# Performance work log

Hardware: AMD Instinct MI355X
Metric: run time of the kernel (lower is better)

The kernel has to match this reference:

```python
import jax, jax.numpy as jnp
import numpy as np
from jax import lax

H_SP, W_SP = 32, 8   # idx == 0
NUM_HEADS = 2
DIM = 64
SCALE = (DIM // NUM_HEADS) ** -0.5


def conv1x1(x, w, b):
    # x: [B,C,H,W], w: [O,C,1,1], b: [O]
    return jnp.einsum('bchw,oc->bohw', x, w[:, :, 0, 0]) + b[None, :, None, None]


def dwconv5(x, w, b):
    # depthwise 5x5, pad 2. w: [C,1,5,5]
    y = lax.conv_general_dilated(
        x, w, window_strides=(1, 1), padding=[(2, 2), (2, 2)],
        dimension_numbers=('NCHW', 'OIHW', 'NCHW'),
        feature_group_count=x.shape[1])
    return y + b[None, :, None, None]


def im2cswin(x):
    # [B,C,H,W] -> [B*nH*nW, heads, H_SP*W_SP, C//heads]
    B, C, H, W = x.shape
    x = x.reshape(B, C, H // H_SP, H_SP, W // W_SP, W_SP)
    x = x.transpose(0, 2, 4, 3, 5, 1).reshape(-1, H_SP * W_SP, NUM_HEADS, C // NUM_HEADS)
    return x.transpose(0, 2, 1, 3)


def windows2img(xw, H, W):
    # [B', H_SP*W_SP, C] -> [B, C, H, W]
    B = xw.shape[0] // ((H // H_SP) * (W // W_SP))
    x = xw.reshape(B, H // H_SP, W // W_SP, H_SP, W_SP, -1)
    return x.transpose(0, 5, 1, 3, 2, 4).reshape(B, -1, H, W)


def setup_inputs() -> dict:
    key = jax.random.key(0)
    ks = jax.random.split(key, 8)
    B, C, H, W = 4, DIM, 256, 256
    s = 0.02
    return {
        'x': jax.random.normal(ks[0], (B, C, H, W), dtype=jnp.float32),
        'qk_w': jax.random.normal(ks[1], (2 * C, C, 1, 1), dtype=jnp.float32) * s,
        'qk_b': jnp.zeros((2 * C,), jnp.float32),
        'q5_w': jax.random.normal(ks[2], (C, 1, 5, 5), dtype=jnp.float32) * s,
        'q5_b': jnp.zeros((C,), jnp.float32),
        'k5_w': jax.random.normal(ks[3], (C, 1, 5, 5), dtype=jnp.float32) * s,
        'k5_b': jnp.zeros((C,), jnp.float32),
        'v_w': jax.random.normal(ks[4], (C, C, 1, 1), dtype=jnp.float32) * s,
        'v_b': jnp.zeros((C,), jnp.float32),
        'lepe_w': jax.random.normal(ks[5], (C, 1, 5, 5), dtype=jnp.float32) * s,
        'lepe_b': jnp.zeros((C,), jnp.float32),
    }


def reference(x, qk_w, qk_b, q5_w, q5_b, k5_w, k5_b, v_w, v_b, lepe_w, lepe_b):
    B, C, H, W = x.shape
    pad_r = (W_SP - W % W_SP) % W_SP
    pad_b = (H_SP - H % H_SP) % H_SP
    xp = jnp.pad(x, ((0, 0), (0, 0), (0, pad_b), (0, pad_r)))
    Hp, Wp = xp.shape[2], xp.shape[3]
    # shift_size == 0 -> no roll
    qk = conv1x1(xp, qk_w, qk_b)
    q, k = jnp.split(qk, 2, axis=1)
    v = conv1x1(xp, v_w, v_b)
    lepe = dwconv5(v, lepe_w, lepe_b)
    qw = im2cswin(dwconv5(q, q5_w, q5_b) + lepe)   # [nw, h, N, d]
    kw = im2cswin(dwconv5(k, k5_w, k5_b) + lepe)
    vw = im2cswin(v)
    attn = jnp.einsum('whnd,whmd->whnm', qw * SCALE, kw)
    attn = jax.nn.softmax(attn, axis=-1)
    out = jnp.einsum('whnm,whmd->whnd', attn, vw)
    out = out.transpose(0, 2, 1, 3).reshape(-1, H_SP * W_SP, C)
    out = windows2img(out, Hp, Wp) + lepe
    if pad_r or pad_b:
        out = out[:, :, :H, :W]
    return out
```

## Files before the change

kernel.cpp:

```cpp
#include <hip/hip_runtime.h>


typedef unsigned short u16;
typedef short s16x8 __attribute__((ext_vector_type(8)));
typedef float f32x4 __attribute__((ext_vector_type(4)));

#define MFMA16(a, b, c) __builtin_amdgcn_mfma_f32_16x16x32_bf16((a), (b), (c), 0, 0, 0)

#define SCALE_F 0.17677669529663687f
#define LOG2E_F 1.4426950408889634f

#if __has_builtin(__builtin_amdgcn_exp2f)
#define EXP2F(x) __builtin_amdgcn_exp2f(x)
#else
#define EXP2F(x) exp2f(x)
#endif

#if __has_builtin(__builtin_amdgcn_rcpf)
#define RCPF(x) __builtin_amdgcn_rcpf(x)
#else
#define RCPF(x) (1.f / (x))
#endif

#if __has_builtin(__builtin_amdgcn_fdot2_f32_bf16)
#define HAVE_DOT2 1
typedef __bf16 bf16x2_t __attribute__((ext_vector_type(2)));
__device__ __forceinline__ float dot2bf(unsigned a, unsigned b, float c) {
  return __builtin_amdgcn_fdot2_f32_bf16(__builtin_bit_cast(bf16x2_t, a),
                                         __builtin_bit_cast(bf16x2_t, b), c,
                                         false);
}
#else
#define HAVE_DOT2 0
#endif

__device__ __forceinline__ u16 f2bf(float f) {
  unsigned u = __float_as_uint(f);
  return (u16)((u + 0x7FFFu + ((u >> 16) & 1u)) >> 16);
}
__device__ __forceinline__ float bf2f(u16 h) {
  return __uint_as_float(((unsigned)h) << 16);
}
__device__ __forceinline__ unsigned pk_rne(float lo, float hi) {
  unsigned ul = __float_as_uint(lo), uh = __float_as_uint(hi);
  ul += 0x7FFFu + ((ul >> 16) & 1u);
  uh += 0x7FFFu + ((uh >> 16) & 1u);
  return (ul >> 16) | (uh & 0xFFFF0000u);
}

__global__ __launch_bounds__(256, 4) void k1_conv1x1(
    const float* __restrict__ x, const float* __restrict__ qk_w,
    const float* __restrict__ qk_b, const float* __restrict__ v_w,
    const float* __restrict__ v_b, u16* __restrict__ qkv) {
  __shared__ u16 Wl[12288];
  __shared__ float Bl[192];
  int t = threadIdx.x;
  for (int i = t; i < 12288; i += 256) {
    int oc = i >> 6, ic = i & 63;
    float wv_ = (oc < 128) ? qk_w[i] : v_w[i - 8192];
    Wl[(oc << 6) | (ic ^ ((oc & 7) << 3))] = f2bf(wv_);
  }
  if (t < 192) Bl[t] = (t < 128) ? qk_b[t] : v_b[t - 128];
  __syncthreads();

  int lane = t & 63, wv = t >> 6;
  int col = lane & 15, g = lane >> 4;
  int p0 = blockIdx.x * 64 + wv * 16;
  int b = p0 >> 16, pix0 = p0 & 65535;

  const float* xb = x + (size_t)b * 4194304 + pix0 + col;
  s16x8 bfrag[2];
#pragma unroll
  for (int kk = 0; kk < 2; ++kk) {
#pragma unroll
    for (int j = 0; j < 8; ++j) {
      int ic = kk * 32 + g * 8 + j;
      bfrag[kk][j] = (short)f2bf(xb[(size_t)ic << 16]);
    }
  }

  f32x4 acc[12];
#pragma unroll
  for (int mt = 0; mt < 12; ++mt) acc[mt] = 0.f;
#pragma unroll
  for (int mt = 0; mt < 12; ++mt) {
    int oc = mt * 16 + col;
    int swz = (oc & 7) << 3;
#pragma unroll
    for (int kk = 0; kk < 2; ++kk) {
      s16x8 af = *(const s16x8*)&Wl[(oc << 6) | ((kk * 32 + g * 8) ^ swz)];
      acc[mt] = MFMA16(af, bfrag[kk], acc[mt]);
    }
  }

  u16* ob = qkv + (size_t)b * 12582912 + pix0 + col;
#pragma unroll
  for (int mt = 0; mt < 12; ++mt) {
#pragma unroll
    for (int r = 0; r < 4; ++r) {
      int oc = mt * 16 + g * 4 + r;
      ob[(size_t)oc << 16] = f2bf(acc[mt][r] + Bl[oc]);
    }
  }
}


__device__ __forceinline__ int qt_off(int tok, int d) {
  return (tok << 5) + (d ^ (((tok >> 2) & 3) << 3));
}
__device__ __forceinline__ int vt_off(int d, int tok) {
  int swz = (((d & 7) ^ ((tok >> 6) & 3)) << 3);
  return (d << 8) + ((tok & ~7) ^ swz) + (tok & 7);
}

template <bool WANTC>
__device__ __forceinline__ void conv25(const u16* hb, const unsigned* ww,
                                       float* acc, unsigned& cA, unsigned& cB) {
#pragma unroll
  for (int i = 0; i < 5; ++i) {
    uint2 A = *(const uint2*)&hb[i * 12];
    uint2 Bv = *(const uint2*)&hb[i * 12 + 4];
    if (WANTC && i == 2) {
      cA = A.y;
      cB = Bv.x;
    }
#if HAVE_DOT2
    unsigned o1 = (A.x >> 16) | (A.y << 16);
    unsigned o3 = (A.y >> 16) | (Bv.x << 16);
    unsigned o5 = (Bv.x >> 16) | (Bv.y << 16);
    unsigned o7 = (Bv.y >> 16) | (Bv.y << 16);
    unsigned pr[8] = {A.x, o1, A.y, o3, Bv.x, o5, Bv.y, o7};
#pragma unroll
    for (int j = 0; j < 4; ++j) {
      float a0 = dot2bf(pr[j], ww[i * 3], acc[j]);
      a0 = dot2bf(pr[j + 2], ww[i * 3 + 1], a0);
      acc[j] = dot2bf(pr[j + 4], ww[i * 3 + 2], a0);
    }
#else
    float px[8];
    px[0] = __uint_as_float(A.x << 16);
    px[1] = __uint_as_float(A.x & 0xffff0000u);
    px[2] = __uint_as_float(A.y << 16);
    px[3] = __uint_as_float(A.y & 0xffff0000u);
    px[4] = __uint_as_float(Bv.x << 16);
    px[5] = __uint_as_float(Bv.x & 0xffff0000u);
    px[6] = __uint_as_float(Bv.y << 16);
    px[7] = __uint_as_float(Bv.y & 0xffff0000u);
    float w5[5];
    w5[0] = __uint_as_float(ww[i * 3] << 16);
    w5[1] = __uint_as_float(ww[i * 3] & 0xffff0000u);
    w5[2] = __uint_as_float(ww[i * 3 + 1] << 16);
    w5[3] = __uint_as_float(ww[i * 3 + 1] & 0xffff0000u);
    w5[4] = __uint_as_float(ww[i * 3 + 2] << 16);
#pragma unroll
    for (int jj = 0; jj < 5; ++jj)
#pragma unroll
      for (int j = 0; j < 4; ++j) acc[j] = fmaf(px[j + jj], w5[jj], acc[j]);
#endif
  }
}

__global__ __launch_bounds__(512, 4) void k23_fused(
    const u16* __restrict__ qkv, const float* __restrict__ q5_w,
    const float* __restrict__ q5_b, const float* __restrict__ k5_w,
    const float* __restrict__ k5_b, const float* __restrict__ lepe_w,
    const float* __restrict__ lepe_b, float* __restrict__ out) {
  __shared__ u16 SM[40256];
  u16* QT = SM;
  u16* KT = SM + 8192;
  u16* VT = SM + 16384;
  u16* LT = SM + 24576;
  u16* HS = SM + 32768;
  unsigned* WLp = (unsigned*)(SM + 36224);
  float* BLf = (float*)(SM + 40064);

  int raw = blockIdx.x;
  int bid = (raw & 7) * 256 + (raw >> 3);
  int head = bid & 1, wj = (bid >> 1) & 31, wi = (bid >> 6) & 7, b = bid >> 9;
  int h0 = wi * 32, w0 = wj * 8;

  int t = threadIdx.x;
  int wv = t >> 6, lane = t & 63;
  int dl = lane & 7, tq = lane >> 3;
  const size_t bbase = (size_t)b * 12582912;

  for (int i = t; i < 1440; i += 512) {
    int ts = i / 480, rem = i - ts * 480, ch = rem / 15, rk = rem - ch * 15;
    int r = rk / 3, k2 = rk - r * 3;
    const float* srcw = (ts == 0 ? lepe_w : ts == 1 ? q5_w : k5_w) +
                        (head * 32 + ch) * 25 + r * 5 + k2 * 2;
    float lo = srcw[0];
    float hi = (k2 < 2) ? srcw[1] : 0.f;
    WLp[ts * 640 + ch * 20 + rk] = pk_rne(lo, hi);
  }
  if (t < 96) {
    int ts = t >> 5, ch = t & 31;
    BLf[t] = (ts == 0 ? lepe_b : ts == 1 ? q5_b : k5_b)[head * 32 + ch];
  }

  unsigned fixOff[4], okm[4];
  int ldsOff[4];
  bool live[4];
#pragma unroll
  for (int it = 0; it < 4; ++it) {
    int ip = t + it * 512;
    live[it] = ip < 1728;
    int ipc = live[it] ? ip : 0;
    int ch = ipc / 216, rem = ipc - ch * 216;
    int hr = rem / 6, hc = rem - hr * 6;
    int gh = h0 - 2 + hr, gw = w0 - 2 + hc * 2;
    bool ok = live[it] & ((unsigned)gh < 256u) & ((unsigned)gw <= 254u);
    int hcl = gh < 0 ? 0 : (gh > 255 ? 255 : gh);
    int wcl = gw < 0 ? 0 : (gw > 254 ? 254 : gw);
    fixOff[it] = ((unsigned)ch << 16) + hcl * 256 + wcl;
    okm[it] = ok ? 0xffffffffu : 0u;
    ldsOff[it] = (ch * 36 + hr) * 12 + hc * 2;
  }

  unsigned crV[4], crQ[4], crK[4];
  auto stage_ld = [&](int p, unsigned* cr) {
    int cg = p / 3, ts = p - cg * 3;
    int planeBase = (ts == 0 ? 128 : ts == 1 ? 0 : 64) + head * 32 + cg * 8;
    const u16* src = qkv + bbase + ((size_t)planeBase << 16);
#pragma unroll
    for (int it = 0; it < 4; ++it)
      if (live[it]) {
        unsigned v = *(const unsigned*)&src[fixOff[it]];
        cr[it] = v & okm[it];
      }
  };
  auto stage_st = [&](const unsigned* cr) {
#pragma unroll
    for (int it = 0; it < 4; ++it)
      if (live[it]) *(unsigned*)&HS[ldsOff[it]] = cr[it];
  };

  stage_ld(0, crV);
  stage_st(crV);
  stage_ld(1, crQ);
  stage_ld(2, crK);
  stage_ld(3, crV);
  __syncthreads();

  int row = wv * 4 + (tq >> 1), c0 = (tq & 1) * 4;
  int tok0 = wv * 32 + tq * 4;
  int hq = tq >> 2;
  int sBv = wv * 32 + (tq & 3) * 8 + hq * 4;
  int qjb = (dl & 1) ? 2 : 0;
  const u16* hb = &HS[(dl * 36 + row) * 12 + c0];
  float lepA[4];

  auto loadw = [&](int ts, int d, unsigned* ww) {
    const uint4* wp = (const uint4*)(WLp + ts * 640 + d * 20);
    uint4 a = wp[0], b4 = wp[1], c4 = wp[2], e4 = wp[3];
    ww[0] = a.x; ww[1] = a.y; ww[2] = a.z; ww[3] = a.w;
    ww[4] = b4.x; ww[5] = b4.y; ww[6] = b4.z; ww[7] = b4.w;
    ww[8] = c4.x; ww[9] = c4.y; ww[10] = c4.z; ww[11] = c4.w;
    ww[12] = e4.x; ww[13] = e4.y; ww[14] = e4.z;
  };

  auto do_qk = [&](const unsigned* ww, float bias, u16* tile, bool doScale,
                   int d) {
    float acc[4] = {bias, bias, bias, bias};
    unsigned du0, du1;
    conv25<false>(hb, ww, acc, du0, du1);
    float o0 = acc[0] + lepA[0], o1 = acc[1] + lepA[1];
    float o2 = acc[2] + lepA[2], o3 = acc[3] + lepA[3];
    if (doScale) {
      o0 *= SCALE_F;
      o1 *= SCALE_F;
      o2 *= SCALE_F;
      o3 *= SCALE_F;
    }
    unsigned q01 = pk_rne(o0, o1), q23 = pk_rne(o2, o3);
    unsigned sendq = (dl & 1) ? q01 : q23;
    unsigned recvq = (unsigned)__shfl_xor((int)sendq, 1);
    unsigned aQ = (dl & 1) ? recvq : q01;
    unsigned bQ = (dl & 1) ? q23 : recvq;
    unsigned wlo = (aQ & 0xffffu) | (bQ << 16);
    unsigned whi = (aQ >> 16) | (bQ & 0xffff0000u);
    int dp = d & ~1;
    unsigned* tw = (unsigned*)tile;
    int wq0 = ((tok0 + qjb) << 4) + ((dp ^ ((tq & 3) << 3)) >> 1);
    tw[wq0] = wlo;
    tw[wq0 + 16] = whi;
  };

#pragma unroll 1
  for (int cg = 0; cg < 4; ++cg) {
    int d = cg * 8 + dl;
    unsigned ww[16];
    loadw(0, d, ww);
    {
      float bias = BLf[d];
      float acc[4] = {bias, bias, bias, bias};
      unsigned cA, cB;
      conv25<true>(hb, ww, acc, cA, cB);
      uint2 ol;
      ol.x = pk_rne(acc[0], acc[1]);
      ol.y = pk_rne(acc[2], acc[3]);
      *(uint2*)&LT[vt_off(d, tok0)] = ol;
      unsigned sendv = hq ? cA : cB;
      unsigned recvv = (unsigned)__shfl_xor((int)sendv, 32);
      unsigned aW = hq ? recvv : cA;
      unsigned bW = hq ? cB : recvv;
      uint2 ov;
      ov.x = (aW & 0xffffu) | (bW << 16);
      ov.y = (aW >> 16) | (bW & 0xffff0000u);
      *(uint2*)&VT[vt_off(d, sBv)] = ov;
#pragma unroll
      for (int j = 0; j < 4; ++j) lepA[j] = acc[j];
    }
    __syncthreads();
    stage_st(crQ);
    if (cg < 3) stage_ld(cg * 3 + 4, crQ);
    __syncthreads();
    loadw(1, d, ww);
    do_qk(ww, BLf[32 + d], QT, true, d);
    __syncthreads();
    stage_st(crK);
    if (cg < 3) stage_ld(cg * 3 + 5, crK);
    __syncthreads();
    loadw(2, d, ww);
    do_qk(ww, BLf[64 + d], KT, false, d);
    __syncthreads();
    if (cg < 3) {
      stage_st(crV);
      if (cg < 2) stage_ld(cg * 3 + 6, crV);
      __syncthreads();
    }
  }

  int col = lane & 15, g = lane >> 4;
  int rbase = wv * 32;

  s16x8 qa[2];
  float lepr[2][8];
#pragma unroll
  for (int mt = 0; mt < 2; ++mt) {
    int tok = rbase + mt * 16 + col;
    qa[mt] = *(const s16x8*)&QT[qt_off(tok, g * 8)];
#pragma unroll
    for (int dt = 0; dt < 2; ++dt)
#pragma unroll
      for (int r = 0; r < 4; ++r) {
        int d = dt * 16 + g * 4 + r;
        lepr[mt][dt * 4 + r] = bf2f(LT[vt_off(d, tok)]);
      }
  }
  __syncthreads();

  u16* Pw = (wv < 4) ? (SM + wv * 2048) : (SM + 24576 + (wv - 4) * 2048);
  float* ob = out + (((size_t)(b * 64 + head * 32)) << 16) + h0 * 256 + w0;

#pragma unroll 1
  for (int mt = 0; mt < 2; ++mt) {
    int row0 = rbase + mt * 16;
    f32x4 zero = 0.f;
    f32x4 sacc[16];
    __builtin_amdgcn_s_setprio(1);
#pragma unroll
    for (int nt = 0; nt < 16; ++nt) {
      int tj = nt * 16 + col;
      s16x8 kb = *(const s16x8*)&KT[qt_off(tj, g * 8)];
      sacc[nt] = MFMA16(qa[mt], kb, zero);
    }
    __builtin_amdgcn_s_setprio(0);
    unsigned pw[4][8];
    float ssum[4];
#pragma unroll
    for (int r = 0; r < 4; ++r) {
      float pv[16];
#pragma unroll
      for (int nt = 0; nt < 16; ++nt) pv[nt] = EXP2F(sacc[nt][r]);
      float s0 = 0.f;
#if HAVE_DOT2
#pragma unroll
      for (int w = 0; w < 8; ++w) {
        pw[r][w] = pk_rne(pv[2 * w], pv[2 * w + 1]);
        s0 = dot2bf(pw[r][w], 0x3F803F80u, s0);
      }
#else
#pragma unroll
      for (int w = 0; w < 8; ++w) {
        pw[r][w] = pk_rne(pv[2 * w], pv[2 * w + 1]);
        s0 += pv[2 * w] + pv[2 * w + 1];
      }
#endif
#pragma unroll
      for (int s = 1; s < 16; s <<= 1) s0 += __shfl_xor(s0, s);
      ssum[r] = s0;
    }
    int srcl = (col >> 2) << 4;
    float t0 = __shfl(ssum[0], srcl);
    float t1 = __shfl(ssum[1], srcl);
    float t2 = __shfl(ssum[2], srcl);
    float t3 = __shfl(ssum[3], srcl);
    float sA = (col & 1) ? t1 : t0;
    float sB = (col & 1) ? t3 : t2;
    float inv = RCPF((col & 2) ? sB : sA);

    f32x4 oacc[2];
    oacc[0] = 0.f;
    oacc[1] = 0.f;
    unsigned* PwU = (unsigned*)Pw;
#pragma unroll
    for (int chunk = 0; chunk < 2; ++chunk) {
#pragma unroll
      for (int r = 0; r < 4; ++r) {
        int irow = g * 4 + r;
        int wb = irow * 64;
        int sw = (irow & 7) << 2;
#pragma unroll
        for (int al = 0; al < 4; ++al)
          PwU[wb + ((al * 16 + col) ^ sw)] = pw[r][chunk * 4 + al];
      }
      __builtin_amdgcn_s_setprio(1);
#pragma unroll
      for (int ks = 0; ks < 4; ++ks) {
        int kcp = (ks * 16 + g * 4) ^ ((col & 7) << 2);
        s16x8 pb = *(const s16x8*)&PwU[col * 64 + kcp];
        int sig = chunk * 128 + ks * 32 + g * 8;
#pragma unroll
        for (int dt = 0; dt < 2; ++dt) {
          s16x8 va = *(const s16x8*)&VT[vt_off(dt * 16 + col, sig)];
          oacc[dt] = MFMA16(va, pb, oacc[dt]);
        }
      }
      __builtin_amdgcn_s_setprio(0);
    }
    int tok = row0 + col;
#pragma unroll
    for (int dt = 0; dt < 2; ++dt) {
#pragma unroll
      for (int r = 0; r < 4; ++r) {
        int d = dt * 16 + g * 4 + r;
        float val = fmaf(oacc[dt][r], inv, lepr[mt][dt * 4 + r]);
        ob[((size_t)d << 16) + (tok >> 3) * 256 + (tok & 7)] = val;
      }
    }
  }
}

extern "C" void kernel_launch(void* const* d_in, const int* in_sizes, int n_in,
                              void* d_out, int out_size, void* d_ws,
                              size_t ws_size, hipStream_t stream) {
  const float* x = (const float*)d_in[0];
  const float* qk_w = (const float*)d_in[1];
  const float* qk_b = (const float*)d_in[2];
  const float* q5_w = (const float*)d_in[3];
  const float* q5_b = (const float*)d_in[4];
  const float* k5_w = (const float*)d_in[5];
  const float* k5_b = (const float*)d_in[6];
  const float* v_w = (const float*)d_in[7];
  const float* v_b = (const float*)d_in[8];
  const float* lepe_w = (const float*)d_in[9];
  const float* lepe_b = (const float*)d_in[10];
  float* out = (float*)d_out;

  if (ws_size < 100663296ull) return;
  u16* qkv = (u16*)d_ws;

  hipLaunchKernelGGL(k1_conv1x1, dim3(4096), dim3(256), 0, stream, x, qk_w,
                     qk_b, v_w, v_b, qkv);
  hipLaunchKernelGGL(k23_fused, dim3(2048), dim3(512), 0, stream, qkv, q5_w,
                     q5_b, k5_w, k5_b, lepe_w, lepe_b, out);
}
```

Measured before the change: 202.7 us.

## Process two horizontally adjacent windows per block and merge their output stores

```diff
diff --git a/kernel.cpp b/kernel.cpp
--- a/kernel.cpp
+++ b/kernel.cpp
@@ -175,9 +175,9 @@
   float* BLf = (float*)(SM + 40064);
 
   int raw = blockIdx.x;
-  int bid = (raw & 7) * 256 + (raw >> 3);
-  int head = bid & 1, wj = (bid >> 1) & 31, wi = (bid >> 6) & 7, b = bid >> 9;
-  int h0 = wi * 32, w0 = wj * 8;
+  int bid = (raw & 7) * 128 + (raw >> 3);
+  int head = bid & 1, wj2 = (bid >> 1) & 15, wi = (bid >> 5) & 7, b = bid >> 8;
+  int h0 = wi * 32, w0A = wj2 * 16;
 
   int t = threadIdx.x;
   int wv = t >> 6, lane = t & 63;
@@ -198,9 +198,9 @@
     BLf[t] = (ts == 0 ? lepe_b : ts == 1 ? q5_b : k5_b)[head * 32 + ch];
   }
 
-  unsigned fixOff[4], okm[4];
-  int ldsOff[4];
-  bool live[4];
+  unsigned ch16[4];
+  int hcs[4], ldsOff[4];
+  bool live[4], okh[4];
 #pragma unroll
   for (int it = 0; it < 4; ++it) {
     int ip = t + it * 512;
@@ -208,39 +208,13 @@
     int ipc = live[it] ? ip : 0;
     int ch = ipc / 216, rem = ipc - ch * 216;
     int hr = rem / 6, hc = rem - hr * 6;
-    int gh = h0 - 2 + hr, gw = w0 - 2 + hc * 2;
-    bool ok = live[it] & ((unsigned)gh < 256u) & ((unsigned)gw <= 254u);
+    int gh = h0 - 2 + hr;
+    okh[it] = live[it] & ((unsigned)gh < 256u);
     int hcl = gh < 0 ? 0 : (gh > 255 ? 255 : gh);
-    int wcl = gw < 0 ? 0 : (gw > 254 ? 254 : gw);
-    fixOff[it] = ((unsigned)ch << 16) + hcl * 256 + wcl;
-    okm[it] = ok ? 0xffffffffu : 0u;
+    ch16[it] = ((unsigned)ch << 16) + hcl * 256;
+    hcs[it] = hc;
     ldsOff[it] = (ch * 36 + hr) * 12 + hc * 2;
   }
-
-  unsigned crV[4], crQ[4], crK[4];
-  auto stage_ld = [&](int p, unsigned* cr) {
-    int cg = p / 3, ts = p - cg * 3;
-    int planeBase = (ts == 0 ? 128 : ts == 1 ? 0 : 64) + head * 32 + cg * 8;
-    const u16* src = qkv + bbase + ((size_t)planeBase << 16);
-#pragma unroll
-    for (int it = 0; it < 4; ++it)
-      if (live[it]) {
-        unsigned v = *(const unsigned*)&src[fixOff[it]];
-        cr[it] = v & okm[it];
-      }
-  };
-  auto stage_st = [&](const unsigned* cr) {
-#pragma unroll
-    for (int it = 0; it < 4; ++it)
-      if (live[it]) *(unsigned*)&HS[ldsOff[it]] = cr[it];
-  };
-
-  stage_ld(0, crV);
-  stage_st(crV);
-  stage_ld(1, crQ);
-  stage_ld(2, crK);
-  stage_ld(3, crV);
-  __syncthreads();
 
   int row = wv * 4 + (tq >> 1), c0 = (tq & 1) * 4;
   int tok0 = wv * 32 + tq * 4;
@@ -248,7 +222,10 @@
   int sBv = wv * 32 + (tq & 3) * 8 + hq * 4;
   int qjb = (dl & 1) ? 2 : 0;
   const u16* hb = &HS[(dl * 36 + row) * 12 + c0];
-  float lepA[4];
+  int col = lane & 15, g = lane >> 4;
+  int rbase = wv * 32;
+  u16* Pw = (wv < 4) ? (SM + wv * 2048) : (SM + 24576 + (wv - 4) * 2048);
+  float* obA = out + (((size_t)(b * 64 + head * 32)) << 16) + h0 * 256 + w0A;
 
   auto loadw = [&](int ts, int d, unsigned* ww) {
     const uint4* wp = (const uint4*)(WLp + ts * 640 + d * 20);
@@ -259,184 +236,230 @@
     ww[12] = e4.x; ww[13] = e4.y; ww[14] = e4.z;
   };
 
-  auto do_qk = [&](const unsigned* ww, float bias, u16* tile, bool doScale,
-                   int d) {
-    float acc[4] = {bias, bias, bias, bias};
-    unsigned du0, du1;
-    conv25<false>(hb, ww, acc, du0, du1);
-    float o0 = acc[0] + lepA[0], o1 = acc[1] + lepA[1];
-    float o2 = acc[2] + lepA[2], o3 = acc[3] + lepA[3];
-    if (doScale) {
-      o0 *= SCALE_F;
-      o1 *= SCALE_F;
-      o2 *= SCALE_F;
-      o3 *= SCALE_F;
-    }
-    unsigned q01 = pk_rne(o0, o1), q23 = pk_rne(o2, o3);
-    unsigned sendq = (dl & 1) ? q01 : q23;
-    unsigned recvq = (unsigned)__shfl_xor((int)sendq, 1);
-    unsigned aQ = (dl & 1) ? recvq : q01;
-    unsigned bQ = (dl & 1) ? q23 : recvq;
-    unsigned wlo = (aQ & 0xffffu) | (bQ << 16);
-    unsigned whi = (aQ >> 16) | (bQ & 0xffff0000u);
-    int dp = d & ~1;
-    unsigned* tw = (unsigned*)tile;
-    int wq0 = ((tok0 + qjb) << 4) + ((dp ^ ((tq & 3) << 3)) >> 1);
-    tw[wq0] = wlo;
-    tw[wq0 + 16] = whi;
-  };
+  float h0v[8], h1v[8];
 
 #pragma unroll 1
-  for (int cg = 0; cg < 4; ++cg) {
-    int d = cg * 8 + dl;
-    unsigned ww[16];
-    loadw(0, d, ww);
-    {
-      float bias = BLf[d];
+  for (int win = 0; win < 2; ++win) {
+    int w0 = w0A + win * 8;
+
+    unsigned fixOff[4], okm[4];
+#pragma unroll
+    for (int it = 0; it < 4; ++it) {
+      int gw = w0 - 2 + hcs[it] * 2;
+      bool ok = okh[it] & ((unsigned)gw <= 254u);
+      int wcl = gw < 0 ? 0 : (gw > 254 ? 254 : gw);
+      fixOff[it] = ch16[it] + wcl;
+      okm[it] = ok ? 0xffffffffu : 0u;
+    }
+
+    unsigned crV[4], crQ[4], crK[4];
+    auto stage_ld = [&](int p, unsigned* cr) {
+      int cg = p / 3, ts = p - cg * 3;
+      int planeBase = (ts == 0 ? 128 : ts == 1 ? 0 : 64) + head * 32 + cg * 8;
+      const u16* src = qkv + bbase + ((size_t)planeBase << 16);
+#pragma unroll
+      for (int it = 0; it < 4; ++it)
+        if (live[it]) {
+          unsigned v = *(const unsigned*)&src[fixOff[it]];
+          cr[it] = v & okm[it];
+        }
+    };
+    auto stage_st = [&](const unsigned* cr) {
+#pragma unroll
+      for (int it = 0; it < 4; ++it)
+        if (live[it]) *(unsigned*)&HS[ldsOff[it]] = cr[it];
+    };
+
+    stage_ld(0, crV);
+    stage_st(crV);
+    stage_ld(1, crQ);
+    stage_ld(2, crK);
+    stage_ld(3, crV);
+    __syncthreads();
+
+    float lepA[4];
+    auto do_qk = [&](const unsigned* ww, float bias, u16* tile, bool doScale,
+                     int d) {
       float acc[4] = {bias, bias, bias, bias};
-      unsigned cA, cB;
-      conv25<true>(hb, ww, acc, cA, cB);
-      uint2 ol;
-      ol.x = pk_rne(acc[0], acc[1]);
-      ol.y = pk_rne(acc[2], acc[3]);
-      *(uint2*)&LT[vt_off(d, tok0)] = ol;
-      unsigned sendv = hq ? cA : cB;
-      unsigned recvv = (unsigned)__shfl_xor((int)sendv, 32);
-      unsigned aW = hq ? recvv : cA;
-      unsigned bW = hq ? cB : recvv;
-      uint2 ov;
-      ov.x = (aW & 0xffffu) | (bW << 16);
-      ov.y = (aW >> 16) | (bW & 0xffff0000u);
-      *(uint2*)&VT[vt_off(d, sBv)] = ov;
-#pragma unroll
-      for (int j = 0; j < 4; ++j) lepA[j] = acc[j];
+      unsigned du0, du1;
+      conv25<false>(hb, ww, acc, du0, du1);
+      float o0 = acc[0] + lepA[0], o1 = acc[1] + lepA[1];
+      float o2 = acc[2] + lepA[2], o3 = acc[3] + lepA[3];
+      if (doScale) {
+        o0 *= SCALE_F;
+        o1 *= SCALE_F;
+        o2 *= SCALE_F;
+        o3 *= SCALE_F;
+      }
+      unsigned q01 = pk_rne(o0, o1), q23 = pk_rne(o2, o3);
+      unsigned sendq = (dl & 1) ? q01 : q23;
+      unsigned recvq = (unsigned)__shfl_xor((int)sendq, 1);
+      unsigned aQ = (dl & 1) ? recvq : q01;
+      unsigned bQ = (dl & 1) ? q23 : recvq;
+      unsigned wlo = (aQ & 0xffffu) | (bQ << 16);
+      unsigned whi = (aQ >> 16) | (bQ & 0xffff0000u);
+      int dp = d & ~1;
+      unsigned* tw = (unsigned*)tile;
+      int wq0 = ((tok0 + qjb) << 4) + ((dp ^ ((tq & 3) << 3)) >> 1);
+      tw[wq0] = wlo;
+      tw[wq0 + 16] = whi;
+    };
+
+#pragma unroll 1
+    for (int cg = 0; cg < 4; ++cg) {
+      int d = cg * 8 + dl;
+      unsigned ww[16];
+      loadw(0, d, ww);
+      {
+        float bias = BLf[d];
+        float acc[4] = {bias, bias, bias, bias};
+        unsigned cA, cB;
+        conv25<true>(hb, ww, acc, cA, cB);
+        uint2 ol;
+        ol.x = pk_rne(acc[0], acc[1]);
+        ol.y = pk_rne(acc[2], acc[3]);
+        *(uint2*)&LT[vt_off(d, tok0)] = ol;
+        unsigned sendv = hq ? cA : cB;
+        unsigned recvv = (unsigned)__shfl_xor((int)sendv, 32);
+        unsigned aW = hq ? recvv : cA;
+        unsigned bW = hq ? cB : recvv;
+        uint2 ov;
+        ov.x = (aW & 0xffffu) | (bW << 16);
+        ov.y = (aW >> 16) | (bW & 0xffff0000u);
+        *(uint2*)&VT[vt_off(d, sBv)] = ov;
+#pragma unroll
+        for (int j = 0; j < 4; ++j) lepA[j] = acc[j];
+      }
+      __syncthreads();
+      stage_st(crQ);
+      if (cg < 3) stage_ld(cg * 3 + 4, crQ);
+      __syncthreads();
+      loadw(1, d, ww);
+      do_qk(ww, BLf[32 + d], QT, true, d);
+      __syncthreads();
+      stage_st(crK);
+      if (cg < 3) stage_ld(cg * 3 + 5, crK);
+      __syncthreads();
+      loadw(2, d, ww);
+      do_qk(ww, BLf[64 + d], KT, false, d);
+      __syncthreads();
+      if (cg < 3) {
+        stage_st(crV);
+        if (cg < 2) stage_ld(cg * 3 + 6, crV);
+        __syncthreads();
+      }
+    }
+
+    s16x8 qa[2];
+    float lepr[2][8];
+#pragma unroll
+    for (int mt = 0; mt < 2; ++mt) {
+      int tok = rbase + mt * 16 + col;
+      qa[mt] = *(const s16x8*)&QT[qt_off(tok, g * 8)];
+#pragma unroll
+      for (int dt = 0; dt < 2; ++dt)
+#pragma unroll
+        for (int r = 0; r < 4; ++r) {
+          int d = dt * 16 + g * 4 + r;
+          lepr[mt][dt * 4 + r] = bf2f(LT[vt_off(d, tok)]);
+        }
     }
     __syncthreads();
-    stage_st(crQ);
-    if (cg < 3) stage_ld(cg * 3 + 4, crQ);
-    __syncthreads();
-    loadw(1, d, ww);
-    do_qk(ww, BLf[32 + d], QT, true, d);
-    __syncthreads();
-    stage_st(crK);
-    if (cg < 3) stage_ld(cg * 3 + 5, crK);
-    __syncthreads();
-    loadw(2, d, ww);
-    do_qk(ww, BLf[64 + d], KT, false, d);
-    __syncthreads();
-    if (cg < 3) {
-      stage_st(crV);
-      if (cg < 2) stage_ld(cg * 3 + 6, crV);
-      __syncthreads();
-    }
-  }
-
-  int col = lane & 15, g = lane >> 4;
-  int rbase = wv * 32;
-
-  s16x8 qa[2];
-  float lepr[2][8];
-#pragma unroll
-  for (int mt = 0; mt < 2; ++mt) {
-    int tok = rbase + mt * 16 + col;
-    qa[mt] = *(const s16x8*)&QT[qt_off(tok, g * 8)];
-#pragma unroll
-    for (int dt = 0; dt < 2; ++dt)
+
+#pragma unroll 1
+    for (int mt = 0; mt < 2; ++mt) {
+      f32x4 zero = 0.f;
+      f32x4 sacc[16];
+      __builtin_amdgcn_s_setprio(1);
+#pragma unroll
+      for (int nt = 0; nt < 16; ++nt) {
+        int tj = nt * 16 + col;
+        s16x8 kb = *(const s16x8*)&KT[qt_off(tj, g * 8)];
+        sacc[nt] = MFMA16(qa[mt], kb, zero);
+      }
+      __builtin_amdgcn_s_setprio(0);
+      unsigned pw[4][8];
+      float ssum[4];
 #pragma unroll
       for (int r = 0; r < 4; ++r) {
-        int d = dt * 16 + g * 4 + r;
-        lepr[mt][dt * 4 + r] = bf2f(LT[vt_off(d, tok)]);
-      }
-  }
-  __syncthreads();
-
-  u16* Pw = (wv < 4) ? (SM + wv * 2048) : (SM + 24576 + (wv - 4) * 2048);
-  float* ob = out + (((size_t)(b * 64 + head * 32)) << 16) + h0 * 256 + w0;
-
-#pragma unroll 1
-  for (int mt = 0; mt < 2; ++mt) {
-    int row0 = rbase + mt * 16;
-    f32x4 zero = 0.f;
-    f32x4 sacc[16];
-    __builtin_amdgcn_s_setprio(1);
-#pragma unroll
-    for (int nt = 0; nt < 16; ++nt) {
-      int tj = nt * 16 + col;
-      s16x8 kb = *(const s16x8*)&KT[qt_off(tj, g * 8)];
-      sacc[nt] = MFMA16(qa[mt], kb, zero);
-    }
-    __builtin_amdgcn_s_setprio(0);
-    unsigned pw[4][8];
-    float ssum[4];
-#pragma unroll
-    for (int r = 0; r < 4; ++r) {
-      float pv[16];
-#pragma unroll
-      for (int nt = 0; nt < 16; ++nt) pv[nt] = EXP2F(sacc[nt][r]);
-      float s0 = 0.f;
+        float pv[16];
+#pragma unroll
+        for (int nt = 0; nt < 16; ++nt) pv[nt] = EXP2F(sacc[nt][r]);
+        float s0 = 0.f;
 #if HAVE_DOT2
 #pragma unroll
-      for (int w = 0; w < 8; ++w) {
-        pw[r][w] = pk_rne(pv[2 * w], pv[2 * w + 1]);
-        s0 = dot2bf(pw[r][w], 0x3F803F80u, s0);
-      }
+        for (int w = 0; w < 8; ++w) {
+          pw[r][w] = pk_rne(pv[2 * w], pv[2 * w + 1]);
+          s0 = dot2bf(pw[r][w], 0x3F803F80u, s0);
+        }
 #else
 #pragma unroll
-      for (int w = 0; w < 8; ++w) {
-        pw[r][w] = pk_rne(pv[2 * w], pv[2 * w + 1]);
-        s0 += pv[2 * w] + pv[2 * w + 1];
-      }
+        for (int w = 0; w < 8; ++w) {
+          pw[r][w] = pk_rne(pv[2 * w], pv[2 * w + 1]);
+          s0 += pv[2 * w] + pv[2 * w + 1];
+        }
 #endif
 #pragma unroll
-      for (int s = 1; s < 16; s <<= 1) s0 += __shfl_xor(s0, s);
-      ssum[r] = s0;
-    }
-    int srcl = (col >> 2) << 4;
-    float t0 = __shfl(ssum[0], srcl);
-    float t1 = __shfl(ssum[1], srcl);
-    float t2 = __shfl(ssum[2], srcl);
-    float t3 = __shfl(ssum[3], srcl);
-    float sA = (col & 1) ? t1 : t0;
-    float sB = (col & 1) ? t3 : t2;
-    float inv = RCPF((col & 2) ? sB : sA);
-
-    f32x4 oacc[2];
-    oacc[0] = 0.f;
-    oacc[1] = 0.f;
-    unsigned* PwU = (unsigned*)Pw;
-#pragma unroll
-    for (int chunk = 0; chunk < 2; ++chunk) {
-#pragma unroll
-      for (int r = 0; r < 4; ++r) {
-        int irow = g * 4 + r;
-        int wb = irow * 64;
-        int sw = (irow & 7) << 2;
-#pragma unroll
-        for (int al = 0; al < 4; ++al)
-          PwU[wb + ((al * 16 + col) ^ sw)] = pw[r][chunk * 4 + al];
-      }
-      __builtin_amdgcn_s_setprio(1);
-#pragma unroll
-      for (int ks = 0; ks < 4; ++ks) {
-        int kcp = (ks * 16 + g * 4) ^ ((col & 7) << 2);
-        s16x8 pb = *(const s16x8*)&PwU[col * 64 + kcp];
-        int sig = chunk * 128 + ks * 32 + g * 8;
-#pragma unroll
-        for (int dt = 0; dt < 2; ++dt) {
-          s16x8 va = *(const s16x8*)&VT[vt_off(dt * 16 + col, sig)];
-          oacc[dt] = MFMA16(va, pb, oacc[dt]);
-        }
-      }
-      __builtin_amdgcn_s_setprio(0);
-    }
-    int tok = row0 + col;
-#pragma unroll
-    for (int dt = 0; dt < 2; ++dt) {
-#pragma unroll
-      for (int r = 0; r < 4; ++r) {
-        int d = dt * 16 + g * 4 + r;
-        float val = fmaf(oacc[dt][r], inv, lepr[mt][dt * 4 + r]);
-        ob[((size_t)d << 16) + (tok >> 3) * 256 + (tok & 7)] = val;
+        for (int s = 1; s < 16; s <<= 1) s0 += __shfl_xor(s0, s);
+        ssum[r] = s0;
+      }
+      int srcl = (col >> 2) << 4;
+      float t0 = __shfl(ssum[0], srcl);
+      float t1 = __shfl(ssum[1], srcl);
+      float t2 = __shfl(ssum[2], srcl);
+      float t3 = __shfl(ssum[3], srcl);
+      float sA = (col & 1) ? t1 : t0;
+      float sB = (col & 1) ? t3 : t2;
+      float inv = RCPF((col & 2) ? sB : sA);
+
+      f32x4 oacc[2];
+      oacc[0] = 0.f;
+      oacc[1] = 0.f;
+      unsigned* PwU = (unsigned*)Pw;
+#pragma unroll
+      for (int chunk = 0; chunk < 2; ++chunk) {
+#pragma unroll
+        for (int r = 0; r < 4; ++r) {
+          int irow = g * 4 + r;
+          int wb = irow * 64;
+          int sw = (irow & 7) << 2;
+#pragma unroll
+          for (int al = 0; al < 4; ++al)
+            PwU[wb + ((al * 16 + col) ^ sw)] = pw[r][chunk * 4 + al];
+        }
+        __builtin_amdgcn_s_setprio(1);
+#pragma unroll
+        for (int ks = 0; ks < 4; ++ks) {
+          int kcp = (ks * 16 + g * 4) ^ ((col & 7) << 2);
+          s16x8 pb = *(const s16x8*)&PwU[col * 64 + kcp];
+          int sig = chunk * 128 + ks * 32 + g * 8;
+#pragma unroll
+          for (int dt = 0; dt < 2; ++dt) {
+            s16x8 va = *(const s16x8*)&VT[vt_off(dt * 16 + col, sig)];
+            oacc[dt] = MFMA16(va, pb, oacc[dt]);
+          }
+        }
+        __builtin_amdgcn_s_setprio(0);
+      }
+      int tok = rbase + mt * 16 + col;
+#pragma unroll
+      for (int dt = 0; dt < 2; ++dt) {
+#pragma unroll
+        for (int r = 0; r < 4; ++r) {
+          int d = dt * 16 + g * 4 + r;
+          float val = fmaf(oacc[dt][r], inv, lepr[mt][dt * 4 + r]);
+          if (win == 0) {
+            if (mt == 0)
+              h0v[dt * 4 + r] = val;
+            else
+              h1v[dt * 4 + r] = val;
+          } else {
+            float hv = (mt == 0) ? h0v[dt * 4 + r] : h1v[dt * 4 + r];
+            size_t off = ((size_t)d << 16) + (tok >> 3) * 256 + (tok & 7);
+            obA[off] = hv;
+            obA[off + 8] = val;
+          }
+        }
       }
     }
   }
@@ -463,6 +486,6 @@
 
   hipLaunchKernelGGL(k1_conv1x1, dim3(4096), dim3(256), 0, stream, x, qk_w,
                      qk_b, v_w, v_b, qkv);
-  hipLaunchKernelGGL(k23_fused, dim3(2048), dim3(512), 0, stream, qkv, q5_w,
+  hipLaunchKernelGGL(k23_fused, dim3(1024), dim3(512), 0, stream, qkv, q5_w,
                      q5_b, k5_w, k5_b, lepe_w, lepe_b, out);
 }
```

Measured after the change: 304.2 us. 1.5x slower.
